# Optimization experiments

Hardware: AMD Instinct MI355X
Metric: run time of the kernel (lower is better)

Reference implementation:

```python
import jax, jax.numpy as jnp
import numpy as np

TOP_RATIO = 0.3
TOP_WEIGHT = 1.0
WEIGHT = 1.0


def setup_inputs() -> dict:
    key = jax.random.key(0)
    k1, k2 = jax.random.split(key)
    pred = jax.random.normal(k1, (8, 20, 512, 1024), dtype=jnp.float32)
    target = jax.random.randint(k2, (8, 512, 1024), 0, 20, dtype=jnp.int64)
    return {"pred": pred, "target": target}


def reference(pred, target):
    # Per-pixel cross entropy: -log_softmax over class dim (axis=1), gathered at target.
    logp = jax.nn.log_softmax(pred, axis=1)                      # [B, C, H, W]
    ce = -jnp.take_along_axis(logp, target[:, None, :, :], axis=1)[:, 0]  # [B, H, W]
    loss_flat = ce.reshape(-1)                                   # [N]
    n = loss_flat.shape[0]                                       # static
    topk_num = int(n * TOP_RATIO)                                # static k
    loss_total = loss_flat.sum() / (n + 1e-12)
    loss_topk, _ = jax.lax.top_k(loss_flat, topk_num)
    loss_total = loss_total + TOP_WEIGHT * loss_topk.mean()
    return loss_total * WEIGHT
```

## Files before the change

kernel.cpp:

```cpp
#include <hip/hip_runtime.h>
#include <stdint.h>

#define NPIX   4194304
#define KSEL   1258291
#define HWSZ   524288
#define NCLS   20

#define CE_BLOCKS 2048
#define HB_BLOCKS 512
#define HB_ITERS  4

#define CBASE  15744
#define NBIN   1536
#define CHUNK  6

#define OFF_H    0
#define MEMSET_LEN 49152
#define OFF_PSUM 49152
#define OFF_CE   65536

typedef float          f4  __attribute__((ext_vector_type(4)));
typedef int            i4  __attribute__((ext_vector_type(4)));
typedef unsigned short us4 __attribute__((ext_vector_type(4)));
typedef unsigned short us8 __attribute__((ext_vector_type(8)));

__device__ __forceinline__ unsigned short f2bf(float x) {
    unsigned u = __float_as_uint(x);
    return (unsigned short)((u + 0x7FFFu + ((u >> 16) & 1u)) >> 16);
}
__device__ __forceinline__ float bf2f(unsigned b) {
    return __uint_as_float(b << 16);
}

__device__ __forceinline__ double block_reduce_d(double d, double* lred) {
    __syncthreads();
    for (int off = 32; off > 0; off >>= 1) d += __shfl_down(d, off);
    int wid  = threadIdx.x >> 6;
    int lane = threadIdx.x & 63;
    if (lane == 0) lred[wid] = d;
    __syncthreads();
    double r = 0.0;
    if (threadIdx.x == 0) {
        for (int i = 0; i < 4; ++i) r += lred[i];
    }
    return r;
}

__global__ __launch_bounds__(256, 4) void ce_kernel(const float* __restrict__ pred,
                                                    const int* __restrict__ tgt,
                                                    unsigned short* __restrict__ ce,
                                                    double* __restrict__ psum) {
    __shared__ double lred[4];
    int t = threadIdx.x, w = t >> 6, l = t & 63;
    int blk = blockIdx.x;
    int g0 = blk << 9;
    int p0 = g0 << 2;
    int b  = p0 >> 19;
    int hw = p0 & (HWSZ - 1);
    const float* base = pred + (size_t)b * (size_t)(NCLS * HWSZ) + hw;

    int go0 = (w << 7) + l;
    int go1 = go0 + 64;

    i4 tt0 = ((const i4*)tgt)[g0 + go0];
    i4 tt1 = ((const i4*)tgt)[g0 + go1];

    float s[8], vt[8];
#pragma unroll
    for (int i = 0; i < 8; ++i) { s[i] = 0.f; vt[i] = 0.f; }

#pragma unroll
    for (int c = 0; c < NCLS; ++c) {
        const f4* pc = (const f4*)(base + (size_t)c * HWSZ);
        f4 a = pc[go0];
        f4 d = pc[go1];
        s[0] += __expf(a.x);
        s[1] += __expf(a.y);
        s[2] += __expf(a.z);
        s[3] += __expf(a.w);
        s[4] += __expf(d.x);
        s[5] += __expf(d.y);
        s[6] += __expf(d.z);
        s[7] += __expf(d.w);
        if (c == tt0.x) vt[0] = a.x;
        if (c == tt0.y) vt[1] = a.y;
        if (c == tt0.z) vt[2] = a.z;
        if (c == tt0.w) vt[3] = a.w;
        if (c == tt1.x) vt[4] = d.x;
        if (c == tt1.y) vt[5] = d.y;
        if (c == tt1.z) vt[6] = d.z;
        if (c == tt1.w) vt[7] = d.w;
    }

    float r[8];
#pragma unroll
    for (int i = 0; i < 8; ++i)
        r[i] = fmaxf(__logf(s[i]) - vt[i], 0.0f);

    us4 u0, u1;
    u0.x = f2bf(r[0]); u0.y = f2bf(r[1]); u0.z = f2bf(r[2]); u0.w = f2bf(r[3]);
    u1.x = f2bf(r[4]); u1.y = f2bf(r[5]); u1.z = f2bf(r[6]); u1.w = f2bf(r[7]);
    ((us4*)ce)[g0 + go0] = u0;
    ((us4*)ce)[g0 + go1] = u1;

    double d = 0.0;
#pragma unroll
    for (int i = 0; i < 8; ++i) d += (double)r[i];
    d = block_reduce_d(d, lred);
    if (t == 0) psum[blk] = d;
}

__global__ __launch_bounds__(256) void hist_kernel(const unsigned short* __restrict__ ce,
                                                   unsigned* __restrict__ h) {
    __shared__ unsigned lh[4][NBIN];
    int t = threadIdx.x, w = t >> 6, blk = blockIdx.x;
    for (int i = t; i < 4 * NBIN; i += 256) ((unsigned*)lh)[i] = 0u;
    __syncthreads();

    const us8* ce8 = (const us8*)ce;
    int tid0 = blk * 256 + t;
#pragma unroll
    for (int it = 0; it < HB_ITERS; ++it) {
        us8 x = ce8[tid0 + it * (HB_BLOCKS * 256)];
#pragma unroll
        for (int j = 0; j < 8; ++j) {
            int bin = (int)(unsigned)x[j] - CBASE;
            bin = (bin < 0) ? 0 : ((bin > NBIN - 1) ? NBIN - 1 : bin);
            atomicAdd(&lh[w][bin], 1u);
        }
    }
    __syncthreads();
    unsigned* hs = h + ((unsigned)blk & 7u) * NBIN;
    for (int i = t; i < NBIN; i += 256) {
        unsigned c = lh[0][i] + lh[1][i] + lh[2][i] + lh[3][i];
        if (c) atomicAdd(&hs[i], c);
    }
}

__global__ __launch_bounds__(256) void fin_kernel(const unsigned* __restrict__ h,
                                                  const double* __restrict__ psum,
                                                  float* __restrict__ out) {
    __shared__ unsigned tmp[256];
    __shared__ unsigned sbin, skrem;
    __shared__ double lred[4];
    int t = threadIdx.x;

    unsigned cnt[CHUNK];
    unsigned lsum = 0;
#pragma unroll
    for (int j = 0; j < CHUNK; ++j) {
        unsigned c = 0;
#pragma unroll
        for (int sdx = 0; sdx < 8; ++sdx) c += h[sdx * NBIN + t * CHUNK + j];
        cnt[j] = c;
        lsum += c;
    }
    tmp[t] = lsum;
    __syncthreads();
    for (int off = 1; off < 256; off <<= 1) {
        unsigned add = (t + off < 256) ? tmp[t + off] : 0u;
        __syncthreads();
        tmp[t] += add;
        __syncthreads();
    }
    unsigned cum = tmp[t] - lsum;
    for (int j = CHUNK - 1; j >= 0; --j) {
        unsigned hv = cnt[j];
        if (cum < (unsigned)KSEL && cum + hv >= (unsigned)KSEL) {
            sbin = (unsigned)(t * CHUNK + j);
            skrem = (unsigned)KSEL - cum;
        }
        cum += hv;
    }
    __syncthreads();
    unsigned b = sbin, krem = skrem;

    double wsum = 0.0;
#pragma unroll
    for (int j = 0; j < CHUNK; ++j) {
        int bin = t * CHUNK + j;
        if (bin > (int)b && cnt[j])
            wsum += (double)cnt[j] * (double)bf2f((unsigned)(bin + CBASE));
    }
    double top = block_reduce_d(wsum, lred);

    double a = 0.0;
    for (int i = t; i < CE_BLOCKS; i += 256) a += psum[i];
    double total = block_reduce_d(a, lred);

    if (t == 0) {
        top += (double)krem * (double)bf2f(b + CBASE);
        double loss = total / ((double)NPIX + 1e-12) + top / (double)KSEL;
        out[0] = (float)loss;
    }
}

extern "C" void kernel_launch(void* const* d_in, const int* in_sizes, int n_in,
                              void* d_out, int out_size, void* d_ws, size_t ws_size,
                              hipStream_t stream) {
    const float* pred = (const float*)d_in[0];
    const int*   tgt  = (const int*)d_in[1];
    float* out = (float*)d_out;
    char* ws = (char*)d_ws;
    unsigned* h    = (unsigned*)(ws + OFF_H);
    double*   psum = (double*)(ws + OFF_PSUM);
    unsigned short* ce = (unsigned short*)(ws + OFF_CE);

    hipMemsetAsync(ws, 0, MEMSET_LEN, stream);
    ce_kernel<<<CE_BLOCKS, 256, 0, stream>>>(pred, tgt, ce, psum);
    hist_kernel<<<HB_BLOCKS, 256, 0, stream>>>(ce, h);
    fin_kernel<<<1, 256, 0, stream>>>(h, psum, out);
}
```

Measured before the change: 81.27 us.

## Fuse histogram construction into cross-entropy kernel, drop bf16 loss buffer

The cross-entropy kernel now bins each per-pixel loss directly into a shared-memory histogram and flushes it to the global histogram copies. This removes the separate histogram kernel and the intermediate bf16 loss array. It avoids writing and rereading that buffer and one kernel launch. In exchange, every one of the 2048 blocks zeroes and flushes 1536 bins, which raises global atomic traffic and LDS use per block.

```diff
diff --git a/kernel.cpp b/kernel.cpp
--- a/kernel.cpp
+++ b/kernel.cpp
@@ -7,8 +7,6 @@
 #define NCLS   20
 
 #define CE_BLOCKS 2048
-#define HB_BLOCKS 512
-#define HB_ITERS  4
 
 #define CBASE  15744
 #define NBIN   1536
@@ -17,12 +15,9 @@
 #define OFF_H    0
 #define MEMSET_LEN 49152
 #define OFF_PSUM 49152
-#define OFF_CE   65536
 
 typedef float          f4  __attribute__((ext_vector_type(4)));
 typedef int            i4  __attribute__((ext_vector_type(4)));
-typedef unsigned short us4 __attribute__((ext_vector_type(4)));
-typedef unsigned short us8 __attribute__((ext_vector_type(8)));
 
 __device__ __forceinline__ unsigned short f2bf(float x) {
     unsigned u = __float_as_uint(x);
@@ -46,12 +41,17 @@
     return r;
 }
 
-__global__ __launch_bounds__(256, 4) void ce_kernel(const float* __restrict__ pred,
-                                                    const int* __restrict__ tgt,
-                                                    unsigned short* __restrict__ ce,
-                                                    double* __restrict__ psum) {
+__global__ __launch_bounds__(256) __attribute__((amdgpu_waves_per_eu(4, 4)))
+void ce_kernel(const float* __restrict__ pred,
+               const int* __restrict__ tgt,
+               double* __restrict__ psum,
+               unsigned* __restrict__ h) {
+    __shared__ unsigned lh[4][NBIN];
     __shared__ double lred[4];
     int t = threadIdx.x, w = t >> 6, l = t & 63;
+    for (int i = t; i < 4 * NBIN; i += 256) ((unsigned*)lh)[i] = 0u;
+    __syncthreads();
+
     int blk = blockIdx.x;
     int g0 = blk << 9;
     int p0 = g0 << 2;
@@ -92,49 +92,24 @@
         if (c == tt1.w) vt[7] = d.w;
     }
 
-    float r[8];
-#pragma unroll
-    for (int i = 0; i < 8; ++i)
-        r[i] = fmaxf(__logf(s[i]) - vt[i], 0.0f);
-
-    us4 u0, u1;
-    u0.x = f2bf(r[0]); u0.y = f2bf(r[1]); u0.z = f2bf(r[2]); u0.w = f2bf(r[3]);
-    u1.x = f2bf(r[4]); u1.y = f2bf(r[5]); u1.z = f2bf(r[6]); u1.w = f2bf(r[7]);
-    ((us4*)ce)[g0 + go0] = u0;
-    ((us4*)ce)[g0 + go1] = u1;
-
     double d = 0.0;
 #pragma unroll
-    for (int i = 0; i < 8; ++i) d += (double)r[i];
-    d = block_reduce_d(d, lred);
-    if (t == 0) psum[blk] = d;
-}
+    for (int i = 0; i < 8; ++i) {
+        float r = fmaxf(__logf(s[i]) - vt[i], 0.0f);
+        d += (double)r;
+        int bin = (int)(unsigned)f2bf(r) - CBASE;
+        bin = (bin < 0) ? 0 : ((bin > NBIN - 1) ? NBIN - 1 : bin);
+        atomicAdd(&lh[w][bin], 1u);
+    }
 
-__global__ __launch_bounds__(256) void hist_kernel(const unsigned short* __restrict__ ce,
-                                                   unsigned* __restrict__ h) {
-    __shared__ unsigned lh[4][NBIN];
-    int t = threadIdx.x, w = t >> 6, blk = blockIdx.x;
-    for (int i = t; i < 4 * NBIN; i += 256) ((unsigned*)lh)[i] = 0u;
-    __syncthreads();
-
-    const us8* ce8 = (const us8*)ce;
-    int tid0 = blk * 256 + t;
-#pragma unroll
-    for (int it = 0; it < HB_ITERS; ++it) {
-        us8 x = ce8[tid0 + it * (HB_BLOCKS * 256)];
-#pragma unroll
-        for (int j = 0; j < 8; ++j) {
-            int bin = (int)(unsigned)x[j] - CBASE;
-            bin = (bin < 0) ? 0 : ((bin > NBIN - 1) ? NBIN - 1 : bin);
-            atomicAdd(&lh[w][bin], 1u);
-        }
-    }
     __syncthreads();
     unsigned* hs = h + ((unsigned)blk & 7u) * NBIN;
     for (int i = t; i < NBIN; i += 256) {
         unsigned c = lh[0][i] + lh[1][i] + lh[2][i] + lh[3][i];
         if (c) atomicAdd(&hs[i], c);
     }
+    d = block_reduce_d(d, lred);
+    if (t == 0) psum[blk] = d;
 }
 
 __global__ __launch_bounds__(256) void fin_kernel(const unsigned* __restrict__ h,
@@ -204,10 +179,8 @@
     char* ws = (char*)d_ws;
     unsigned* h    = (unsigned*)(ws + OFF_H);
     double*   psum = (double*)(ws + OFF_PSUM);
-    unsigned short* ce = (unsigned short*)(ws + OFF_CE);
 
     hipMemsetAsync(ws, 0, MEMSET_LEN, stream);
-    ce_kernel<<<CE_BLOCKS, 256, 0, stream>>>(pred, tgt, ce, psum);
-    hist_kernel<<<HB_BLOCKS, 256, 0, stream>>>(ce, h);
+    ce_kernel<<<CE_BLOCKS, 256, 0, stream>>>(pred, tgt, psum, h);
     fin_kernel<<<1, 256, 0, stream>>>(h, psum, out);
 }
```

Result: faster. 76.21 us (median of 2 runs) (-6.2%).
